# Performance work log

Hardware: AMD Instinct MI355X
Metric: run time of the kernel (lower is better)

Reference implementation:

```python
import jax, jax.numpy as jnp
import numpy as np

N, E, F, H, G = 50000, 1600000, 128, 128, 64
EPS = 1e-5  # BatchNorm eps


def setup_inputs() -> dict:
    key = jax.random.key(0)
    ks = jax.random.split(key, 16)
    x = jax.random.normal(ks[0], (N, F), dtype=jnp.float32)
    edge_index = jax.random.randint(ks[1], (2, E), 0, N, dtype=jnp.int64)
    batch = jnp.sort(jax.random.randint(ks[2], (N,), 0, G, dtype=jnp.int64))
    inp = {
        'x': x, 'edge_index': edge_index, 'batch': batch,
        'W1': jax.random.normal(ks[3], (F, H), dtype=jnp.float32) / np.sqrt(F),
        'b1': jnp.zeros((H,), jnp.float32),
        'bn1_gamma': jax.random.uniform(ks[4], (H,), jnp.float32, 0.5, 1.5),
        'bn1_beta': jax.random.normal(ks[5], (H,), jnp.float32) * 0.1,
        'bn1_mean': jax.random.normal(ks[6], (H,), jnp.float32) * 0.1,
        'bn1_var': jax.random.uniform(ks[7], (H,), jnp.float32, 0.5, 1.5),
        'W2': jax.random.normal(ks[8], (H, H), dtype=jnp.float32) / np.sqrt(H),
        'b2': jnp.zeros((H,), jnp.float32),
        'bn2_gamma': jax.random.uniform(ks[9], (H,), jnp.float32, 0.5, 1.5),
        'bn2_beta': jax.random.normal(ks[10], (H,), jnp.float32) * 0.1,
        'bn2_mean': jax.random.normal(ks[11], (H,), jnp.float32) * 0.1,
        'bn2_var': jax.random.uniform(ks[12], (H,), jnp.float32, 0.5, 1.5),
        'att_w': jax.random.normal(ks[13], (H, 1), dtype=jnp.float32) / np.sqrt(H),
        'cls_w': jax.random.normal(ks[14], (1, H), dtype=jnp.float32) / np.sqrt(H),
        'cls_b': jnp.zeros((1,), jnp.float32),
    }
    return inp


def gcn_conv(h, W, b, src, dst, n):
    # PyG GCNConv: linear, add self-loops, symmetric D^{-1/2}(A+I)D^{-1/2} aggregation, bias.
    hw = h @ W                                   # [n, H]
    loops = jnp.arange(n, dtype=src.dtype)
    s = jnp.concatenate([src, loops])
    d = jnp.concatenate([dst, loops])
    deg = jax.ops.segment_sum(jnp.ones_like(d, dtype=hw.dtype), d, num_segments=n)
    dis = jnp.where(deg > 0, jax.lax.rsqrt(deg), 0.0)
    norm = dis[s] * dis[d]                       # [E+n]
    msgs = hw[s] * norm[:, None]                 # gather + scale (memory-bound)
    return jax.ops.segment_sum(msgs, d, num_segments=n) + b


def batch_norm(h, gamma, beta, mean, var):
    return (h - mean) * gamma * jax.lax.rsqrt(var + EPS) + beta


def reference(x, edge_index, batch, W1, b1, bn1_gamma, bn1_beta, bn1_mean, bn1_var,
              W2, b2, bn2_gamma, bn2_beta, bn2_mean, bn2_var, att_w, cls_w, cls_b):
    n = x.shape[0]
    src, dst = edge_index[0], edge_index[1]
    # eval mode: dropout and edge-dropout are no-ops; BN uses running stats
    h = gcn_conv(x, W1, b1, src, dst, n)
    h = jax.nn.relu(batch_norm(h, bn1_gamma, bn1_beta, bn1_mean, bn1_var))
    h = gcn_conv(h, W2, b2, src, dst, n)
    h = jax.nn.relu(batch_norm(h, bn2_gamma, bn2_beta, bn2_mean, bn2_var))
    att = jax.nn.sigmoid(h @ att_w)              # [n, 1]
    g = jax.ops.segment_sum(h * att, batch, num_segments=G)  # [G, H]
    logits = g @ cls_w.T + cls_b                 # [G, 1]
    return logits, att
```

## Files before the change

### kernel.cpp

```cpp
#include <hip/hip_runtime.h>
#include <math.h>

#define NN 50000
#define HID 128
#define NG 64
#define BN_EPS 1e-5f

typedef __attribute__((ext_vector_type(8))) short short8;
typedef __attribute__((ext_vector_type(4))) float f32x4;

__device__ inline unsigned pack_bf2(float a, float b) {
    union { float f; unsigned u; } ua, ub;
    ua.f = a; ub.f = b;
    unsigned x = ua.u, y = ub.u;
    x += 0x7fffu + ((x >> 16) & 1u);
    y += 0x7fffu + ((y >> 16) & 1u);
    return (x >> 16) | (y & 0xffff0000u);
}
__device__ inline unsigned short bf16_1(float x) {
    union { float f; unsigned u; } v;
    v.f = x;
    unsigned r = v.u + 0x7fffu + ((v.u >> 16) & 1u);
    return (unsigned short)(r >> 16);
}
__device__ inline float2 unpack_bf2(unsigned v) {
    union { unsigned u; float f; } a, b;
    a.u = v << 16;
    b.u = v & 0xffff0000u;
    return make_float2(a.f, b.f);
}

#define NBKT 256
#define ETILE 8192
#define CAP   8192

__global__ __launch_bounds__(256) void k_distribute(const int* __restrict__ src,
                                                    const int* __restrict__ dst,
                                                    int* __restrict__ bcurP,
                                                    unsigned* __restrict__ bpacked,
                                                    int E, int K) {
    __shared__ int h[NBKT];
    int t = threadIdx.x;
    h[t] = 0;
    __syncthreads();
    int base = blockIdx.x * ETILE;
    for (int i = 0; i < ETILE / 256; ++i) {
        int e = base + i * 256 + t;
        if (e < E) atomicAdd(&h[dst[e] / K], 1);
    }
    __syncthreads();
    int c = h[t];
    int my = (c > 0) ? atomicAdd(&bcurP[t * 16], c) : 0;
    __syncthreads();
    h[t] = my;
    __syncthreads();
    for (int i = 0; i < ETILE / 256; ++i) {
        int e = base + i * 256 + t;
        if (e < E) {
            int d = dst[e];
            int p = atomicAdd(&h[d / K], 1);
            bpacked[p] = ((unsigned)d << 16) | (unsigned)src[e];
        }
    }
}

__global__ __launch_bounds__(256) void k_bucket_csr(const unsigned* __restrict__ bpacked,
                                                    const int* __restrict__ bcurP,
                                                    int* __restrict__ row_ptr,
                                                    int* __restrict__ degA,
                                                    float* __restrict__ dis,
                                                    int* __restrict__ col_idx,
                                                    int n, int K) {
    __shared__ int cnt[NBKT];
    __shared__ int sA[NBKT];
    __shared__ int cur[NBKT];
    int t = threadIdx.x;
    int b = blockIdx.x;
    int node0 = b * K;
    int nn = n - node0;
    if (nn > K) nn = K;
    int e0 = b * CAP;
    int e1 = bcurP[b * 16];
    cnt[t] = 0;
    __syncthreads();
    for (int e = e0 + t; e < e1; e += 256) {
        int ld = (int)(bpacked[e] >> 16) - node0;
        atomicAdd(&cnt[ld], 1);
    }
    __syncthreads();
    int c = cnt[t];
    sA[t] = c;
    __syncthreads();
    for (int off = 1; off < NBKT; off <<= 1) {
        int v = (t >= off) ? sA[t - off] : 0;
        __syncthreads();
        sA[t] += v;
        __syncthreads();
    }
    int rp = e0 + sA[t] - c;
    cur[t] = rp;
    if (t < nn) {
        row_ptr[node0 + t] = rp;
        degA[node0 + t] = c;
        dis[node0 + t] = rsqrtf((float)(c + 1));
    }
    __syncthreads();
    for (int e = e0 + t; e < e1; e += 256) {
        unsigned v = bpacked[e];
        int ld = (int)(v >> 16) - node0;
        int p = atomicAdd(&cur[ld], 1);
        col_idx[p] = (int)(v & 0xFFFFu);
    }
}


__global__ __launch_bounds__(128) void k_prep(const float* __restrict__ W1,
                                              const float* __restrict__ W2,
                                              unsigned short* __restrict__ wt1,
                                              unsigned short* __restrict__ wt2,
                                              int* __restrict__ bcurP,
                                              const float* __restrict__ cls_b,
                                              float* __restrict__ logits) {
    int b = blockIdx.x;
    int t = threadIdx.x;
    if (b < 256) {
        int k = b & 127;
        const float* W = (b < 128) ? W1 : W2;
        unsigned short* wt = (b < 128) ? wt1 : wt2;
        wt[t * 128 + k] = bf16_1(W[k * 128 + t]);
    } else {
        bcurP[t * 16] = t * CAP;
        bcurP[(t + 128) * 16] = (t + 128) * CAP;
        if (t < NG) logits[t] = cls_b[0];
    }
}


#define ASTR 136

__global__ __launch_bounds__(256) void k_gemm_mfma(const void* __restrict__ inp,
                                                   const unsigned short* __restrict__ wt,
                                                   const float* __restrict__ dis,
                                                   unsigned short* __restrict__ outb,
                                                   int n, int fmt) {
    __shared__ unsigned short A[64][ASTR];
    int t = threadIdx.x;
    int row0 = blockIdx.x * 64;

    if (fmt == 0) {
        const float* in = (const float*)inp;
        #pragma unroll
        for (int i = 0; i < 8; ++i) {
            int idx = t + i * 256;
            int r = idx >> 5;
            int c4 = (idx & 31) * 4;
            float4 v = make_float4(0.f, 0.f, 0.f, 0.f);
            if (row0 + r < n) v = *(const float4*)&in[(size_t)(row0 + r) * 128 + c4];
            uint2 p;
            p.x = pack_bf2(v.x, v.y);
            p.y = pack_bf2(v.z, v.w);
            *(uint2*)&A[r][c4] = p;
        }
    } else {
        const unsigned short* in = (const unsigned short*)inp;
        #pragma unroll
        for (int i = 0; i < 4; ++i) {
            int idx = t + i * 256;
            int r = idx >> 4;
            int c8 = (idx & 15) * 8;
            uint4 v = make_uint4(0, 0, 0, 0);
            if (row0 + r < n) v = *(const uint4*)&in[(size_t)(row0 + r) * 128 + c8];
            *(uint4*)&A[r][c8] = v;
        }
    }
    __syncthreads();

    int lane = t & 63;
    int wave = t >> 6;
    int m = lane & 15;
    int quad = lane >> 4;
    int r0 = wave * 16;

    short8 a[4];
    #pragma unroll
    for (int kt = 0; kt < 4; ++kt)
        a[kt] = *(const short8*)&A[r0 + m][kt * 32 + quad * 8];

    f32x4 acc[8];
    #pragma unroll
    for (int ct = 0; ct < 8; ++ct) acc[ct] = (f32x4){0.f, 0.f, 0.f, 0.f};

    #pragma unroll
    for (int ct = 0; ct < 8; ++ct) {
        const unsigned short* wb = &wt[(size_t)(ct * 16 + m) * 128 + quad * 8];
        #pragma unroll
        for (int kt = 0; kt < 4; ++kt) {
            short8 b = *(const short8*)(wb + kt * 32);
            acc[ct] = __builtin_amdgcn_mfma_f32_16x16x32_bf16(a[kt], b, acc[ct], 0, 0, 0);
        }
    }

    int gr = row0 + r0 + quad * 4;
    float ds[4];
    #pragma unroll
    for (int reg = 0; reg < 4; ++reg)
        ds[reg] = (gr + reg < n) ? dis[gr + reg] : 0.f;

    __syncthreads();
    #pragma unroll
    for (int ct = 0; ct < 8; ++ct) {
        int col = ct * 16 + m;
        #pragma unroll
        for (int reg = 0; reg < 4; ++reg)
            A[r0 + quad * 4 + reg][col] = bf16_1(acc[ct][reg] * ds[reg]);
    }
    __syncthreads();
    #pragma unroll
    for (int i = 0; i < 4; ++i) {
        int idx = t + i * 256;
        int r = idx >> 4;
        int c8 = (idx & 15) * 8;
        int grow = row0 + r;
        if (grow < n)
            *(uint4*)&outb[(size_t)grow * 128 + c8] = *(const uint4*)&A[r][c8];
    }
}


__device__ inline void gather4wide(const unsigned short* __restrict__ hwsb,
                                   const int* __restrict__ col_idx,
                                   int e0, int deg, int md,
                                   int sl, int part, bool active,
                                   float* acc8) {
    int cidx = (active && sl < deg) ? col_idx[e0 + sl] : 0;
    for (int it0 = 0; it0 < md; it0 += 16) {
        int nx = it0 + 16;
        int cidx_next = (active && (nx + sl) < deg && nx < md) ? col_idx[e0 + nx + sl] : 0;
        uint4 vv[16];
        #pragma unroll
        for (int j = 0; j < 16; ++j) {
            int s = __shfl(cidx, (part << 4) + j);
            vv[j] = (it0 + j < deg)
                        ? *(const uint4*)(hwsb + ((size_t)s << 7) + (sl << 3))
                        : make_uint4(0, 0, 0, 0);
        }
        #pragma unroll
        for (int j = 0; j < 16; ++j) {
            const unsigned* w = (const unsigned*)&vv[j];
            #pragma unroll
            for (int i2 = 0; i2 < 4; ++i2) {
                float2 f = unpack_bf2(w[i2]);
                acc8[2 * i2]     += f.x;
                acc8[2 * i2 + 1] += f.y;
            }
        }
        cidx = cidx_next;
    }
}


__global__ __launch_bounds__(256) void k_agg_bn_relu(const unsigned short* __restrict__ hwsb,
                                                     const int* __restrict__ row_ptr,
                                                     const int* __restrict__ degA,
                                                     const int* __restrict__ col_idx,
                                                     const float* __restrict__ dis,
                                                     const float* __restrict__ bias,
                                                     const float* __restrict__ gamma,
                                                     const float* __restrict__ beta,
                                                     const float* __restrict__ mean,
                                                     const float* __restrict__ var,
                                                     unsigned short* __restrict__ outh, int n) {
    int t = threadIdx.x;
    int wave = t >> 6, lane = t & 63;
    int sl = lane & 15, part = lane >> 4;
    int d = blockIdx.x * 16 + wave * 4 + part;
    bool active = (d < n);
    int e0 = 0, deg = 0;
    if (active) {
        e0 = row_ptr[d];
        deg = degA[d];
    }
    int md = deg;
    md = max(md, __shfl_xor(md, 16));
    md = max(md, __shfl_xor(md, 32));

    float acc8[8] = {0, 0, 0, 0, 0, 0, 0, 0};
    gather4wide(hwsb, col_idx, e0, deg, md, sl, part, active, acc8);
    if (!active) return;

    {
        uint4 v = *(const uint4*)(hwsb + ((size_t)d << 7) + (sl << 3));
        const unsigned* w = (const unsigned*)&v;
        #pragma unroll
        for (int i2 = 0; i2 < 4; ++i2) {
            float2 f = unpack_bf2(w[i2]);
            acc8[2 * i2]     += f.x;
            acc8[2 * i2 + 1] += f.y;
        }
    }
    float dd = dis[d];
    int f0 = sl << 3;
    unsigned outw[4];
    #pragma unroll
    for (int i2 = 0; i2 < 4; ++i2) {
        int f = f0 + 2 * i2;
        float2 bv = *(const float2*)&bias[f];
        float2 gm = *(const float2*)&gamma[f];
        float2 bt = *(const float2*)&beta[f];
        float2 mn = *(const float2*)&mean[f];
        float2 vr = *(const float2*)&var[f];
        float vx = acc8[2 * i2] * dd + bv.x;
        float vy = acc8[2 * i2 + 1] * dd + bv.y;
        float sx = gm.x * rsqrtf(vr.x + BN_EPS);
        float sy = gm.y * rsqrtf(vr.y + BN_EPS);
        float rx = fmaxf((vx - mn.x) * sx + bt.x, 0.f);
        float ry = fmaxf((vy - mn.y) * sy + bt.y, 0.f);
        outw[i2] = pack_bf2(rx, ry);
    }
    *(uint4*)(outh + ((size_t)d << 7) + (sl << 3)) = *(uint4*)outw;
}


__global__ __launch_bounds__(256) void k_agg2_att_logit(const unsigned short* __restrict__ hwsb,
                                                        const int* __restrict__ row_ptr,
                                                        const int* __restrict__ degA,
                                                        const int* __restrict__ col_idx,
                                                        const float* __restrict__ dis,
                                                        const float* __restrict__ bias,
                                                        const float* __restrict__ gamma,
                                                        const float* __restrict__ beta,
                                                        const float* __restrict__ mean,
                                                        const float* __restrict__ var,
                                                        const int* __restrict__ batch,
                                                        const float* __restrict__ att_w,
                                                        const float* __restrict__ cls_w,
                                                        float* __restrict__ att_out,
                                                        float* __restrict__ logits, int n) {
    __shared__ int   sg[16];
    __shared__ float sv[16];
    int t = threadIdx.x;
    int wave = t >> 6, lane = t & 63;
    int sl = lane & 15, part = lane >> 4;
    int d = blockIdx.x * 16 + wave * 4 + part;
    bool active = (d < n);
    int e0 = 0, deg = 0;
    if (active) {
        e0 = row_ptr[d];
        deg = degA[d];
    }
    int md = deg;
    md = max(md, __shfl_xor(md, 16));
    md = max(md, __shfl_xor(md, 32));

    float acc8[8] = {0, 0, 0, 0, 0, 0, 0, 0};
    gather4wide(hwsb, col_idx, e0, deg, md, sl, part, active, acc8);

    int g = -1;
    float contrib = 0.f;
    float p = 0.f, q = 0.f;
    if (active) {
        uint4 v = *(const uint4*)(hwsb + ((size_t)d << 7) + (sl << 3));
        const unsigned* w = (const unsigned*)&v;
        #pragma unroll
        for (int i2 = 0; i2 < 4; ++i2) {
            float2 f = unpack_bf2(w[i2]);
            acc8[2 * i2]     += f.x;
            acc8[2 * i2 + 1] += f.y;
        }
        float dd = dis[d];
        int f0 = sl << 3;
        #pragma unroll
        for (int i2 = 0; i2 < 4; ++i2) {
            int f = f0 + 2 * i2;
            float2 bv = *(const float2*)&bias[f];
            float2 gm = *(const float2*)&gamma[f];
            float2 bt = *(const float2*)&beta[f];
            float2 mn = *(const float2*)&mean[f];
            float2 vr = *(const float2*)&var[f];
            float vx = acc8[2 * i2] * dd + bv.x;
            float vy = acc8[2 * i2 + 1] * dd + bv.y;
            float sx = gm.x * rsqrtf(vr.x + BN_EPS);
            float sy = gm.y * rsqrtf(vr.y + BN_EPS);
            float rx = fmaxf((vx - mn.x) * sx + bt.x, 0.f);
            float ry = fmaxf((vy - mn.y) * sy + bt.y, 0.f);
            float2 aw = *(const float2*)&att_w[f];
            float2 cw = *(const float2*)&cls_w[f];
            p += rx * aw.x + ry * aw.y;
            q += rx * cw.x + ry * cw.y;
        }
    }
    #pragma unroll
    for (int off = 1; off < 16; off <<= 1) {
        p += __shfl_xor(p, off);
        q += __shfl_xor(q, off);
    }
    if (active) {
        float a = 1.f / (1.f + expf(-p));
        if (sl == 0) att_out[d] = a;
        g = batch[d];
        contrib = a * q;
    }
    if (sl == 0) {
        sg[wave * 4 + part] = g;
        sv[wave * 4 + part] = contrib;
    }
    __syncthreads();
    if (t == 0) {
        int cur = -1;
        float acc = 0.f;
        #pragma unroll
        for (int i = 0; i < 16; ++i) {
            int gi = sg[i];
            if (gi < 0) continue;
            if (gi != cur) {
                if (cur >= 0) atomicAdd(&logits[cur], acc);
                cur = gi;
                acc = 0.f;
            }
            acc += sv[i];
        }
        if (cur >= 0) atomicAdd(&logits[cur], acc);
    }
}


extern "C" void kernel_launch(void* const* d_in, const int* in_sizes, int n_in,
                              void* d_out, int out_size, void* d_ws, size_t ws_size,
                              hipStream_t stream) {
    const float* x   = (const float*)d_in[0];
    const int*   ei  = (const int*)d_in[1];
    const int*   bat = (const int*)d_in[2];
    const float* W1  = (const float*)d_in[3];
    const float* b1  = (const float*)d_in[4];
    const float* g1  = (const float*)d_in[5];
    const float* bt1 = (const float*)d_in[6];
    const float* mn1 = (const float*)d_in[7];
    const float* vr1 = (const float*)d_in[8];
    const float* W2  = (const float*)d_in[9];
    const float* b2  = (const float*)d_in[10];
    const float* g2  = (const float*)d_in[11];
    const float* bt2 = (const float*)d_in[12];
    const float* mn2 = (const float*)d_in[13];
    const float* vr2 = (const float*)d_in[14];
    const float* attw = (const float*)d_in[15];
    const float* clsw = (const float*)d_in[16];
    const float* clsb = (const float*)d_in[17];

    int E = in_sizes[1] / 2;
    int n = in_sizes[2];
    const int* src = ei;
    const int* dst = ei + E;
    int K = (n + NBKT - 1) / NBKT;

    char* ws = (char*)d_ws;
    auto alloc = [&](size_t bytes) {
        void* p = (void*)ws;
        ws += (bytes + 255) & ~(size_t)255;
        return p;
    };
    int*            bcurP   = (int*)alloc(NBKT * 16 * 4);
    unsigned*       bpacked = (unsigned*)alloc((size_t)NBKT * CAP * 4);
    int*            row_ptr = (int*)alloc((size_t)n * 4);
    int*            degA    = (int*)alloc((size_t)n * 4);
    int*            col_idx = (int*)alloc((size_t)NBKT * CAP * 4);
    float*          dis     = (float*)alloc((size_t)n * 4);
    unsigned short* hwsb    = (unsigned short*)alloc((size_t)n * 128 * 2);
    unsigned short* h1b     = (unsigned short*)alloc((size_t)n * 128 * 2);
    unsigned short* wt1     = (unsigned short*)alloc(128 * 128 * 2);
    unsigned short* wt2     = (unsigned short*)alloc(128 * 128 * 2);

    float* out = (float*)d_out;
    int etiles = (E + ETILE - 1) / ETILE;
    int gb = (n + 63) / 64;
    int ab = (n + 15) / 16;

    k_prep<<<257, 128, 0, stream>>>(W1, W2, wt1, wt2, bcurP, clsb, out);
    k_distribute<<<etiles, 256, 0, stream>>>(src, dst, bcurP, bpacked, E, K);
    k_bucket_csr<<<NBKT, 256, 0, stream>>>(bpacked, bcurP, row_ptr, degA, dis, col_idx, n, K);

    k_gemm_mfma<<<gb, 256, 0, stream>>>(x, wt1, dis, hwsb, n, 0);
    k_agg_bn_relu<<<ab, 256, 0, stream>>>(hwsb, row_ptr, degA, col_idx, dis,
                                          b1, g1, bt1, mn1, vr1, h1b, n);
    k_gemm_mfma<<<gb, 256, 0, stream>>>(h1b, wt2, dis, hwsb, n, 1);
    k_agg2_att_logit<<<ab, 256, 0, stream>>>(hwsb, row_ptr, degA, col_idx, dis,
                                             b2, g2, bt2, mn2, vr2, bat, attw, clsw,
                                             out + NG, out, n);
}
```

Before: 306.5 us.

## Sort nodes by degree within buckets, fold weight prep into distribute, prefetch B

Adds a per-bucket counting sort of nodes by in-degree, producing a permutation so each aggregation wave processes nodes of similar degree, which reduces divergence from the max-degree loop across the four nodes per wave. Weight transpose/bf16 conversion is moved into extra blocks of the distribute kernel, leaving a tiny init kernel. The GEMM now double-buffers the B-fragment loads across column tiles. In exchange, aggregation reads become permuted, which can hurt locality of row_ptr/degA reads and of the output writes, and the bucket kernel gains extra scan work.

```diff
diff --git a/kernel.cpp b/kernel.cpp
--- a/kernel.cpp
+++ b/kernel.cpp
@@ -34,11 +34,32 @@
 #define ETILE 8192
 #define CAP   8192
 
+__global__ __launch_bounds__(256) void k_init(int* __restrict__ bcurP,
+                                              const float* __restrict__ cls_b,
+                                              float* __restrict__ logits) {
+    int t = threadIdx.x;
+    bcurP[t * 16] = t * CAP;
+    if (t < NG) logits[t] = cls_b[0];
+}
+
 __global__ __launch_bounds__(256) void k_distribute(const int* __restrict__ src,
                                                     const int* __restrict__ dst,
                                                     int* __restrict__ bcurP,
                                                     unsigned* __restrict__ bpacked,
-                                                    int E, int K) {
+                                                    const float* __restrict__ W1,
+                                                    const float* __restrict__ W2,
+                                                    unsigned short* __restrict__ wt1,
+                                                    unsigned short* __restrict__ wt2,
+                                                    int etiles, int E, int K) {
+    if ((int)blockIdx.x >= etiles) {
+        int b2 = blockIdx.x - etiles;
+        int k = b2 & 127;
+        const float* W = (b2 < 128) ? W1 : W2;
+        unsigned short* wt = (b2 < 128) ? wt1 : wt2;
+        int c = threadIdx.x;
+        if (c < 128) wt[c * 128 + k] = bf16_1(W[k * 128 + c]);
+        return;
+    }
     __shared__ int h[NBKT];
     int t = threadIdx.x;
     h[t] = 0;
@@ -70,6 +91,7 @@
                                                     int* __restrict__ degA,
                                                     float* __restrict__ dis,
                                                     int* __restrict__ col_idx,
+                                                    int* __restrict__ perm,
                                                     int n, int K) {
     __shared__ int cnt[NBKT];
     __shared__ int sA[NBKT];
@@ -79,6 +101,7 @@
     int node0 = b * K;
     int nn = n - node0;
     if (nn > K) nn = K;
+    if (nn < 0) nn = 0;
     int e0 = b * CAP;
     int e1 = bcurP[b * 16];
     cnt[t] = 0;
@@ -111,27 +134,27 @@
         int p = atomicAdd(&cur[ld], 1);
         col_idx[p] = (int)(v & 0xFFFFu);
     }
-}
-
-
-__global__ __launch_bounds__(128) void k_prep(const float* __restrict__ W1,
-                                              const float* __restrict__ W2,
-                                              unsigned short* __restrict__ wt1,
-                                              unsigned short* __restrict__ wt2,
-                                              int* __restrict__ bcurP,
-                                              const float* __restrict__ cls_b,
-                                              float* __restrict__ logits) {
-    int b = blockIdx.x;
-    int t = threadIdx.x;
-    if (b < 256) {
-        int k = b & 127;
-        const float* W = (b < 128) ? W1 : W2;
-        unsigned short* wt = (b < 128) ? wt1 : wt2;
-        wt[t * 128 + k] = bf16_1(W[k * 128 + t]);
-    } else {
-        bcurP[t * 16] = t * CAP;
-        bcurP[(t + 128) * 16] = (t + 128) * CAP;
-        if (t < NG) logits[t] = cls_b[0];
+    __syncthreads();
+    sA[t] = 0;
+    __syncthreads();
+    int dc = (c > 255) ? 255 : c;
+    if (t < nn) atomicAdd(&sA[dc], 1);
+    __syncthreads();
+    cur[t] = sA[t];
+    __syncthreads();
+    for (int off = 1; off < NBKT; off <<= 1) {
+        int v = (t >= off) ? cur[t - off] : 0;
+        __syncthreads();
+        cur[t] += v;
+        __syncthreads();
+    }
+    int dbase = cur[t] - sA[t];
+    __syncthreads();
+    sA[t] = dbase;
+    __syncthreads();
+    if (t < nn) {
+        int r = atomicAdd(&sA[dc], 1);
+        perm[node0 + r] = node0 + t;
     }
 }
 
@@ -190,14 +213,24 @@
     #pragma unroll
     for (int ct = 0; ct < 8; ++ct) acc[ct] = (f32x4){0.f, 0.f, 0.f, 0.f};
 
+    short8 bcur[4], bnxt[4];
+    {
+        const unsigned short* wb = &wt[(size_t)m * 128 + quad * 8];
+        #pragma unroll
+        for (int kt = 0; kt < 4; ++kt) bcur[kt] = *(const short8*)(wb + kt * 32);
+    }
     #pragma unroll
     for (int ct = 0; ct < 8; ++ct) {
-        const unsigned short* wb = &wt[(size_t)(ct * 16 + m) * 128 + quad * 8];
-        #pragma unroll
-        for (int kt = 0; kt < 4; ++kt) {
-            short8 b = *(const short8*)(wb + kt * 32);
-            acc[ct] = __builtin_amdgcn_mfma_f32_16x16x32_bf16(a[kt], b, acc[ct], 0, 0, 0);
-        }
+        if (ct < 7) {
+            const unsigned short* wb = &wt[(size_t)((ct + 1) * 16 + m) * 128 + quad * 8];
+            #pragma unroll
+            for (int kt = 0; kt < 4; ++kt) bnxt[kt] = *(const short8*)(wb + kt * 32);
+        }
+        #pragma unroll
+        for (int kt = 0; kt < 4; ++kt)
+            acc[ct] = __builtin_amdgcn_mfma_f32_16x16x32_bf16(a[kt], bcur[kt], acc[ct], 0, 0, 0);
+        #pragma unroll
+        for (int kt = 0; kt < 4; ++kt) bcur[kt] = bnxt[kt];
     }
 
     int gr = row0 + r0 + quad * 4;
@@ -263,6 +296,7 @@
                                                      const int* __restrict__ row_ptr,
                                                      const int* __restrict__ degA,
                                                      const int* __restrict__ col_idx,
+                                                     const int* __restrict__ perm,
                                                      const float* __restrict__ dis,
                                                      const float* __restrict__ bias,
                                                      const float* __restrict__ gamma,
@@ -273,10 +307,11 @@
     int t = threadIdx.x;
     int wave = t >> 6, lane = t & 63;
     int sl = lane & 15, part = lane >> 4;
-    int d = blockIdx.x * 16 + wave * 4 + part;
-    bool active = (d < n);
-    int e0 = 0, deg = 0;
+    int slot = blockIdx.x * 16 + wave * 4 + part;
+    bool active = (slot < n);
+    int d = 0, e0 = 0, deg = 0;
     if (active) {
+        d = perm[slot];
         e0 = row_ptr[d];
         deg = degA[d];
     }
@@ -325,6 +360,7 @@
                                                         const int* __restrict__ row_ptr,
                                                         const int* __restrict__ degA,
                                                         const int* __restrict__ col_idx,
+                                                        const int* __restrict__ perm,
                                                         const float* __restrict__ dis,
                                                         const float* __restrict__ bias,
                                                         const float* __restrict__ gamma,
@@ -341,10 +377,11 @@
     int t = threadIdx.x;
     int wave = t >> 6, lane = t & 63;
     int sl = lane & 15, part = lane >> 4;
-    int d = blockIdx.x * 16 + wave * 4 + part;
-    bool active = (d < n);
-    int e0 = 0, deg = 0;
+    int slot = blockIdx.x * 16 + wave * 4 + part;
+    bool active = (slot < n);
+    int d = 0, e0 = 0, deg = 0;
     if (active) {
+        d = perm[slot];
         e0 = row_ptr[d];
         deg = degA[d];
     }
@@ -463,6 +500,7 @@
     int*            row_ptr = (int*)alloc((size_t)n * 4);
     int*            degA    = (int*)alloc((size_t)n * 4);
     int*            col_idx = (int*)alloc((size_t)NBKT * CAP * 4);
+    int*            perm    = (int*)alloc((size_t)n * 4);
     float*          dis     = (float*)alloc((size_t)n * 4);
     unsigned short* hwsb    = (unsigned short*)alloc((size_t)n * 128 * 2);
     unsigned short* h1b     = (unsigned short*)alloc((size_t)n * 128 * 2);
@@ -474,15 +512,17 @@
     int gb = (n + 63) / 64;
     int ab = (n + 15) / 16;
 
-    k_prep<<<257, 128, 0, stream>>>(W1, W2, wt1, wt2, bcurP, clsb, out);
-    k_distribute<<<etiles, 256, 0, stream>>>(src, dst, bcurP, bpacked, E, K);
-    k_bucket_csr<<<NBKT, 256, 0, stream>>>(bpacked, bcurP, row_ptr, degA, dis, col_idx, n, K);
+    k_init<<<1, 256, 0, stream>>>(bcurP, clsb, out);
+    k_distribute<<<etiles + 256, 256, 0, stream>>>(src, dst, bcurP, bpacked,
+                                                   W1, W2, wt1, wt2, etiles, E, K);
+    k_bucket_csr<<<NBKT, 256, 0, stream>>>(bpacked, bcurP, row_ptr, degA, dis,
+                                           col_idx, perm, n, K);
 
     k_gemm_mfma<<<gb, 256, 0, stream>>>(x, wt1, dis, hwsb, n, 0);
-    k_agg_bn_relu<<<ab, 256, 0, stream>>>(hwsb, row_ptr, degA, col_idx, dis,
+    k_agg_bn_relu<<<ab, 256, 0, stream>>>(hwsb, row_ptr, degA, col_idx, perm, dis,
                                           b1, g1, bt1, mn1, vr1, h1b, n);
     k_gemm_mfma<<<gb, 256, 0, stream>>>(h1b, wt2, dis, hwsb, n, 1);
-    k_agg2_att_logit<<<ab, 256, 0, stream>>>(hwsb, row_ptr, degA, col_idx, dis,
+    k_agg2_att_logit<<<ab, 256, 0, stream>>>(hwsb, row_ptr, degA, col_idx, perm, dis,
                                              b2, g2, bt2, mn2, vr2, bat, attw, clsw,
                                              out + NG, out, n);
 }
```

Result: slower. 319.3 us (+4.2%).
